# Optimization experiments

Measured on AMD Instinct MI355X. Metric: run time of the kernel, lower is better.

Reference implementation:

```python
import jax, jax.numpy as jnp
import numpy as np

EMBED = 1024
HEADS = 16
HEAD_DIM = EMBED // HEADS
NEG = -1e20


def setup_inputs() -> dict:
    key = jax.random.key(0)
    ks = jax.random.split(key, 12)
    N, S, E = 2, 2048, EMBED
    w = lambda k: (jax.random.normal(k, (E, E), dtype=jnp.float32) * 0.02)
    b = lambda k: (jax.random.normal(k, (E,), dtype=jnp.float32) * 0.02)
    return {
        "values": jax.random.normal(ks[0], (N, S, E), dtype=jnp.float32),
        "keys": jax.random.normal(ks[1], (N, S, E), dtype=jnp.float32),
        "query": jax.random.normal(ks[2], (N, S, E), dtype=jnp.float32),
        "mask": jnp.ones((N, S), dtype=jnp.int32),
        "Wv": w(ks[3]), "bv": b(ks[4]),
        "Wk": w(ks[5]), "bk": b(ks[6]),
        "Wq": w(ks[7]), "bq": b(ks[8]),
        "Wo": w(ks[9]), "bo": b(ks[10]),
    }


def reference(values, keys, query, mask, Wv, bv, Wk, bk, Wq, bq, Wo, bo):
    N, S, E = query.shape
    # torch nn.Linear: x @ W.T + b
    v = (values @ Wv.T + bv).reshape(N, S, HEADS, HEAD_DIM)
    k = (keys @ Wk.T + bk).reshape(N, S, HEADS, HEAD_DIM)
    q = (query @ Wq.T + bq).reshape(N, S, HEADS, HEAD_DIM)
    # full [N,H,Q,K] score matrix, as in the original einsum
    energy = jnp.einsum('nqhd,nkhd->nhqk', q, k)
    # 2D mask with mismatched dims triggers causal tril path in the original
    causal = jnp.tril(jnp.ones((S, S), dtype=bool))  # [Q,K]
    energy = jnp.where(causal[None, None, :, :], energy, NEG)
    # NOTE: original scales by sqrt(embed_size), not sqrt(head_dim)
    attn = jax.nn.softmax(energy / jnp.sqrt(jnp.float32(E)), axis=3)
    out = jnp.einsum('nhqk,nkhd->nqhd', attn, v).reshape(N, S, E)
    return out @ Wo.T + bo
```

## Files before the change

kernel.cpp:

```cpp
#include <hip/hip_runtime.h>

typedef __bf16 bf16;
typedef __bf16 bf16x4 __attribute__((ext_vector_type(4)));
typedef __bf16 bf16x8 __attribute__((ext_vector_type(8)));
typedef float floatx4 __attribute__((ext_vector_type(4)));

#define GLOAD_LDS16(gp, lp) \
  __builtin_amdgcn_global_load_lds( \
      (const __attribute__((address_space(1))) void*)(gp), \
      (__attribute__((address_space(3))) void*)(lp), 16, 0, 0)

__global__ __launch_bounds__(256) void cvt_all_kernel(
    const float* __restrict__ v, const float* __restrict__ k, const float* __restrict__ q,
    const float* __restrict__ wv, const float* __restrict__ wk,
    const float* __restrict__ wq, const float* __restrict__ wo,
    bf16* __restrict__ xv, bf16* __restrict__ xk, bf16* __restrict__ xq,
    bf16* __restrict__ bwv, bf16* __restrict__ bwk, bf16* __restrict__ bwq,
    bf16* __restrict__ bwo) {
  const int i = blockIdx.x * 256 + threadIdx.x;
  const int A4 = 1 << 20;
  const float* src; bf16* dst; int off;
  if (i < A4)            { src = v; dst = xv; off = i; }
  else if (i < 2 * A4)   { src = k; dst = xk; off = i - A4; }
  else if (i < 3 * A4)   { src = q; dst = xq; off = i - 2 * A4; }
  else {
    int j = i - 3 * A4; int r = j >> 18; off = j & ((1 << 18) - 1);
    src = (r == 0) ? wv : (r == 1) ? wk : (r == 2) ? wq : wo;
    dst = (r == 0) ? bwv : (r == 1) ? bwk : (r == 2) ? bwq : bwo;
  }
  float4 x = reinterpret_cast<const float4*>(src)[off];
  union { bf16 b[4]; short4 s; } u;
  u.b[0] = (bf16)x.x; u.b[1] = (bf16)x.y; u.b[2] = (bf16)x.z; u.b[3] = (bf16)x.w;
  reinterpret_cast<short4*>(dst)[off] = u.s;
}

template <int MODE>
__device__ __forceinline__ void gemm_body(
    const bf16* __restrict__ A, const bf16* __restrict__ B,
    const float* __restrict__ bias, void* __restrict__ Cout,
    int bx, int by, bf16* __restrict__ SMEM) {
  constexpr int K = 1024, N = 1024;
  constexpr int NSTEP = K / 32;
  const int tid = threadIdx.x;
  const int lane = tid & 63;
  const int wave = tid >> 6;
  const int quad = lane >> 4;
  const int l16 = lane & 15;
  const int wm = (wave >> 1) * 64;
  const int wn = (wave & 1) * 64;
  const int am0 = by * 128;
  const int bn0 = bx * 128;
  const int srow = lane >> 2;
  const int scol = (lane & 3) * 8;

  floatx4 acc[4][4] = {};

  auto stage = [&](int step, int bufsel) {
    const int k0 = step * 32;
    bf16* As = SMEM + bufsel * 8192;
    bf16* Bs = As + 4096;
#pragma unroll
    for (int j = 0; j < 2; j++) {
      const int chunk = wave * 2 + j;
      const int row = chunk * 16 + srow;
      GLOAD_LDS16(A + (size_t)(am0 + row) * K + k0 + scol, As + chunk * 512);
      GLOAD_LDS16(B + (size_t)(bn0 + row) * K + k0 + scol, Bs + chunk * 512);
    }
  };

  auto compute = [&](int bufsel) {
    const bf16* As = SMEM + bufsel * 8192;
    const bf16* Bs = As + 4096;
    bf16x8 af[4], bfv[4];
#pragma unroll
    for (int mi = 0; mi < 4; mi++)
      af[mi] = *reinterpret_cast<const bf16x8*>(&As[(wm + mi * 16 + l16) * 32 + quad * 8]);
#pragma unroll
    for (int ni = 0; ni < 4; ni++)
      bfv[ni] = *reinterpret_cast<const bf16x8*>(&Bs[(wn + ni * 16 + l16) * 32 + quad * 8]);
#pragma unroll
    for (int mi = 0; mi < 4; mi++)
#pragma unroll
      for (int ni = 0; ni < 4; ni++)
        acc[mi][ni] = __builtin_amdgcn_mfma_f32_16x16x32_bf16(af[mi], bfv[ni], acc[mi][ni], 0, 0, 0);
  };

  stage(0, 0);
  for (int t = 0; t < NSTEP; t += 2) {
    __syncthreads();
    stage(t + 1, 1);
    compute(0);
    __syncthreads();
    if (t + 2 < NSTEP) stage(t + 2, 0);
    compute(1);
  }

  if constexpr (MODE == 2) {
#pragma unroll
    for (int mi = 0; mi < 4; mi++) {
#pragma unroll
      for (int ni = 0; ni < 4; ni++) {
        const int col = bn0 + wn + ni * 16 + l16;
        const float bb = bias[col];
        const int row = am0 + wm + mi * 16 + quad * 4;
#pragma unroll
        for (int r = 0; r < 4; r++)
          reinterpret_cast<float*>(Cout)[(size_t)(row + r) * N + col] = acc[mi][ni][r] + bb;
      }
    }
  } else {
    __syncthreads();
    bf16* T = SMEM + wave * 2048;
    const int nb = (am0 + wm) >> 11;
    const int sq0 = (am0 + wm) & 2047;
    const int h = (bn0 + wn) >> 6;
    const int nh = nb * 16 + h;
    const int r8 = lane >> 3, c8 = lane & 7;

    if constexpr (MODE == 0) {
#pragma unroll
      for (int pp = 0; pp < 2; pp++) {
#pragma unroll
        for (int mm = 0; mm < 2; mm++) {
          const int mi = pp * 2 + mm;
#pragma unroll
          for (int ni = 0; ni < 4; ni++) {
            const int d = ni * 16 + l16;
            const float bc = bias[bn0 + wn + d];
#pragma unroll
            for (int r = 0; r < 4; r++) {
              const int s = mm * 16 + quad * 4 + r;
              T[s * 64 + (d & 7) + 8 * ((d >> 3) ^ (s & 7))] = (bf16)(acc[mi][ni][r] + bc);
            }
          }
        }
#pragma unroll
        for (int it = 0; it < 4; it++) {
          const int s = it * 8 + r8;
          bf16x8 vv = *reinterpret_cast<const bf16x8*>(&T[s * 64 + ((c8 ^ r8) * 8)]);
          *reinterpret_cast<bf16x8*>(
              reinterpret_cast<bf16*>(Cout) +
              ((size_t)nh * 2048 + sq0 + pp * 32 + s) * 64 + c8 * 8) = vv;
        }
      }
    } else {
#pragma unroll
      for (int pp = 0; pp < 2; pp++) {
#pragma unroll
        for (int nn = 0; nn < 2; nn++) {
          const int ni = pp * 2 + nn;
          const int dp = nn * 16 + l16;
          const float bc = bias[bn0 + wn + pp * 32 + dp];
#pragma unroll
          for (int mi = 0; mi < 4; mi++) {
#pragma unroll
            for (int r = 0; r < 4; r++) {
              const int s = mi * 16 + quad * 4 + r;
              T[dp * 64 + (s & 7) + 8 * ((s >> 3) ^ (dp & 7))] = (bf16)(acc[mi][ni][r] + bc);
            }
          }
        }
#pragma unroll
        for (int it = 0; it < 4; it++) {
          const int dp = it * 8 + r8;
          bf16x8 vv = *reinterpret_cast<const bf16x8*>(&T[dp * 64 + ((c8 ^ r8) * 8)]);
          *reinterpret_cast<bf16x8*>(
              reinterpret_cast<bf16*>(Cout) +
              ((size_t)nh * 64 + pp * 32 + dp) * 2048 + sq0 + c8 * 8) = vv;
        }
      }
    }
  }
}

__global__ __launch_bounds__(256) void gemm_qkv(
    const bf16* __restrict__ A0, const bf16* __restrict__ B0, const float* __restrict__ c0, bf16* __restrict__ C0,
    const bf16* __restrict__ A1, const bf16* __restrict__ B1, const float* __restrict__ c1, bf16* __restrict__ C1,
    const bf16* __restrict__ A2, const bf16* __restrict__ B2, const float* __restrict__ c2, bf16* __restrict__ C2) {
  extern __shared__ __align__(16) bf16 SMEM[];
  const int lin = blockIdx.x + (blockIdx.y << 3) + (blockIdx.z << 8);
  const int swz = (lin & 7) * 96 + (lin >> 3);
  const int bz = swz >> 8;
  const int by = (swz >> 3) & 31;
  const int bx = swz & 7;
  if (bz == 0)      gemm_body<0>(A0, B0, c0, C0, bx, by, SMEM);
  else if (bz == 1) gemm_body<0>(A1, B1, c1, C1, bx, by, SMEM);
  else              gemm_body<1>(A2, B2, c2, C2, bx, by, SMEM);
}

__global__ __launch_bounds__(256) void gemm_out(
    const bf16* __restrict__ A, const bf16* __restrict__ B,
    const float* __restrict__ bias, float* __restrict__ C) {
  extern __shared__ __align__(16) bf16 SMEM[];
  const int lin = blockIdx.x + (blockIdx.y << 3);
  const int swz = (lin & 7) * 32 + (lin >> 3);
  const int by = swz >> 3;
  const int bx = swz & 7;
  gemm_body<2>(A, B, bias, C, bx, by, SMEM);
}

#define S_LEN 2048
#define EMB 1024
#define QT 128
#define KTILE 64
#define SCALE2 (0.03125f * 1.44269504f)

__global__ __launch_bounds__(256) void attn_kernel(
    const bf16* __restrict__ Qh, const bf16* __restrict__ Kh,
    const bf16* __restrict__ Vt, bf16* __restrict__ O,
    float* __restrict__ Opart, float* __restrict__ lpart) {
  __shared__ __align__(16) bf16 Ks[2 * KTILE * 64];
  __shared__ __align__(16) bf16 Vs[2 * 64 * KTILE];

  const int tid = threadIdx.x;
  const int lane = tid & 63;
  const int wave = tid >> 6;
  const int quad = lane >> 4;
  const int l16 = lane & 15;
  const int wq = wave * 32;

  const int c = blockIdx.x;
  const int role = blockIdx.y;
  const int nh = c >> 3;
  const int t = c & 7;
  const int n = nh >> 4;
  const int h = nh & 15;
  int qt, kt0, kt1;
  if (role == 0) { qt = t; kt0 = 0; kt1 = 2 * t + 2; }
  else {
    qt = 15 - t;
    const int halfk = qt + 1;
    kt0 = (role == 1) ? 0 : halfk;
    kt1 = (role == 1) ? halfk : 2 * halfk;
  }
  const int q0 = qt * QT;

  bf16x8 aq[2][2];
  {
    const bf16* Qb = Qh + ((size_t)nh * S_LEN + q0 + wq + l16) * 64 + quad * 8;
#pragma unroll
    for (int mi = 0; mi < 2; mi++)
#pragma unroll
      for (int kc = 0; kc < 2; kc++)
        aq[mi][kc] = *reinterpret_cast<const bf16x8*>(Qb + mi * 16 * 64 + kc * 32);
  }

  float l_part[2] = {};
  floatx4 o_acc[2][4] = {};

  const bf16* Kbase = Kh + (size_t)nh * S_LEN * 64;
  const bf16* Vbase = Vt + (size_t)nh * 64 * S_LEN;

  const int srl = lane >> 3;
  const int sc8 = lane & 7;

  auto stage = [&](int kt) {
    const int k0s = kt * KTILE;
    const int buf = (kt & 1) * 4096;
#pragma unroll
    for (int j = 0; j < 2; j++) {
      const int rl = wave * 16 + j * 8 + srl;
      const int c8s = ((sc8 ^ (rl & 7)) * 8);
      GLOAD_LDS16(Kbase + (size_t)(k0s + rl) * 64 + c8s, Ks + buf + (wave * 16 + j * 8) * 64);
      GLOAD_LDS16(Vbase + (size_t)rl * S_LEN + k0s + c8s, Vs + buf + (wave * 16 + j * 8) * 64);
    }
  };

  stage(kt0);
  for (int kt = kt0; kt < kt1; kt++) {
    const int k0 = kt * KTILE;
    __syncthreads();
    if (kt + 1 < kt1) stage(kt + 1);
    const bf16* Kc = Ks + (kt & 1) * 4096;
    const bf16* Vc = Vs + (kt & 1) * 4096;

    floatx4 s_acc[2][4] = {};
#pragma unroll
    for (int kc = 0; kc < 2; kc++) {
      bf16x8 bk[4];
#pragma unroll
      for (int ni = 0; ni < 4; ni++)
        bk[ni] = *reinterpret_cast<const bf16x8*>(
            &Kc[(ni * 16 + l16) * 64 + (((kc * 4 + quad) ^ (l16 & 7)) * 8)]);
#pragma unroll
      for (int mi = 0; mi < 2; mi++)
#pragma unroll
        for (int ni = 0; ni < 4; ni++)
          s_acc[mi][ni] = __builtin_amdgcn_mfma_f32_16x16x32_bf16(bk[ni], aq[mi][kc], s_acc[mi][ni], 0, 0, 0);
    }

    const bool needMask = (k0 + KTILE - 1) > (q0 + wq);
    const int qg = q0 + wq + l16;
    union PU { bf16x8 w[2]; bf16x4 q[4]; };
    PU P[2];
#pragma unroll
    for (int mi = 0; mi < 2; mi++) {
#pragma unroll
      for (int ni = 0; ni < 4; ni++) {
        const int kgb = k0 + ni * 16 + quad * 4;
        bf16x4 pk;
#pragma unroll
        for (int r = 0; r < 4; r++) {
          float pr = __builtin_amdgcn_exp2f(s_acc[mi][ni][r] * SCALE2);
          if (needMask) pr = ((kgb + r) <= (qg + mi * 16)) ? pr : 0.f;
          l_part[mi] += pr;
          pk[r] = (bf16)pr;
        }
        P[mi].q[ni] = pk;
      }
    }

#pragma unroll
    for (int kc = 0; kc < 2; kc++) {
      bf16x8 bv[4];
#pragma unroll
      for (int di = 0; di < 4; di++) {
        const bf16* base = Vc + (di * 16 + l16) * 64;
        const int e = l16 & 7;
        union VU { bf16x8 v8; bf16x4 h[2]; } vu;
        vu.h[0] = *reinterpret_cast<const bf16x4*>(
            base + (((kc * 4 + (quad >> 1)) ^ e) * 8) + (quad & 1) * 4);
        vu.h[1] = *reinterpret_cast<const bf16x4*>(
            base + (((kc * 4 + 2 + (quad >> 1)) ^ e) * 8) + (quad & 1) * 4);
        bv[di] = vu.v8;
      }
#pragma unroll
      for (int mi = 0; mi < 2; mi++)
#pragma unroll
        for (int di = 0; di < 4; di++)
          o_acc[mi][di] = __builtin_amdgcn_mfma_f32_16x16x32_bf16(P[mi].w[kc], bv[di], o_acc[mi][di], 0, 0, 0);
    }
  }

  float l_sum[2];
#pragma unroll
  for (int mi = 0; mi < 2; mi++) {
    float s = l_part[mi];
    s += __shfl_xor(s, 16);
    s += __shfl_xor(s, 32);
    l_sum[mi] = s;
  }

  if (role == 0) {
    bf16* Op = O + ((size_t)(n * S_LEN + q0 + wq)) * EMB + h * 64;
#pragma unroll
    for (int mi = 0; mi < 2; mi++) {
      const float linv = 1.0f / l_sum[mi];
#pragma unroll
      for (int r = 0; r < 4; r++) {
        const float inv = __shfl(linv, quad * 4 + r);
        bf16* orow = Op + (size_t)(mi * 16 + quad * 4 + r) * EMB;
#pragma unroll
        for (int di = 0; di < 4; di++)
          orow[di * 16 + l16] = (bf16)(o_acc[mi][di][r] * inv);
      }
    }
  } else {
    float* Ob = Opart + ((size_t)c * 2 + (role - 1)) * (QT * 64);
    float* lb = lpart + ((size_t)c * 2 + (role - 1)) * QT;
#pragma unroll
    for (int mi = 0; mi < 2; mi++)
      if (lane < 16) lb[wq + mi * 16 + lane] = l_sum[mi];
#pragma unroll
    for (int mi = 0; mi < 2; mi++)
#pragma unroll
      for (int r = 0; r < 4; r++) {
        float* orow = Ob + (size_t)(wq + mi * 16 + quad * 4 + r) * 64;
#pragma unroll
        for (int di = 0; di < 4; di++)
          orow[di * 16 + l16] = o_acc[mi][di][r];
      }
  }
}

__global__ __launch_bounds__(256) void attn_combine(
    const float* __restrict__ Opart, const float* __restrict__ lpart,
    bf16* __restrict__ O) {
  const int c = blockIdx.x;
  const int nh = c >> 3;
  const int t = c & 7;
  const int qt = 15 - t;
  const int n = nh >> 4;
  const int h = nh & 15;
  const float* O1 = Opart + (size_t)c * 2 * (QT * 64);
  const float* O2 = O1 + QT * 64;
  const float* l1 = lpart + (size_t)c * 2 * QT;
  const float* l2 = l1 + QT;
  const int tid = threadIdx.x;
  for (int i = tid; i < QT * 64 / 4; i += 256) {
    const int row = i >> 4;
    const float inv = 1.0f / (l1[row] + l2[row]);
    float4 a = reinterpret_cast<const float4*>(O1)[i];
    float4 b = reinterpret_cast<const float4*>(O2)[i];
    bf16x4 pk;
    pk[0] = (bf16)((a.x + b.x) * inv);
    pk[1] = (bf16)((a.y + b.y) * inv);
    pk[2] = (bf16)((a.z + b.z) * inv);
    pk[3] = (bf16)((a.w + b.w) * inv);
    *reinterpret_cast<bf16x4*>(
        O + ((size_t)(n * S_LEN + qt * QT + row)) * EMB + h * 64 + (i & 15) * 4) = pk;
  }
}

extern "C" void kernel_launch(void* const* d_in, const int* in_sizes, int n_in,
                              void* d_out, int out_size, void* d_ws, size_t ws_size,
                              hipStream_t stream) {
  (void)in_sizes; (void)n_in; (void)out_size; (void)ws_size;
  const float* values = (const float*)d_in[0];
  const float* keys   = (const float*)d_in[1];
  const float* query  = (const float*)d_in[2];
  const float* Wv = (const float*)d_in[4];
  const float* bv = (const float*)d_in[5];
  const float* Wk = (const float*)d_in[6];
  const float* bk = (const float*)d_in[7];
  const float* Wq = (const float*)d_in[8];
  const float* bq = (const float*)d_in[9];
  const float* Wo = (const float*)d_in[10];
  const float* bo = (const float*)d_in[11];
  float* out = (float*)d_out;

  const int S = 2048, E = 1024;
  const int M = 2 * S;
  const size_t MB_ = 1u << 20;
  char* ws = (char*)d_ws;
  bf16* xv  = (bf16*)(ws + 0 * MB_);
  bf16* xk  = (bf16*)(ws + 8 * MB_);
  bf16* xq  = (bf16*)(ws + 16 * MB_);
  bf16* wvb = (bf16*)(ws + 24 * MB_);
  bf16* wkb = (bf16*)(ws + 26 * MB_);
  bf16* wqb = (bf16*)(ws + 28 * MB_);
  bf16* wob = (bf16*)(ws + 30 * MB_);
  bf16* kh  = (bf16*)(ws + 32 * MB_);
  bf16* qh  = (bf16*)(ws + 40 * MB_);
  bf16* vt  = (bf16*)(ws + 48 * MB_);
  bf16* ao  = (bf16*)(ws + 56 * MB_);
  float* Opart = (float*)(ws + 0 * MB_);
  float* lpart = (float*)(ws + 17 * MB_);

  cvt_all_kernel<<<(4 << 20) / 256, 256, 0, stream>>>(
      values, keys, query, Wv, Wk, Wq, Wo,
      xv, xk, xq, wvb, wkb, wqb, wob);

  gemm_qkv<<<dim3(E / 128, M / 128, 3), 256, 32768, stream>>>(
      xq, wqb, bq, qh,
      xk, wkb, bk, kh,
      xv, wvb, bv, vt);

  attn_kernel<<<dim3(256, 3), 256, 0, stream>>>(qh, kh, vt, ao, Opart, lpart);
  attn_combine<<<dim3(256), 256, 0, stream>>>(Opart, lpart, ao);

  gemm_out<<<dim3(E / 128, M / 128), 256, 32768, stream>>>(ao, wob, bo, out);
}
```

Measured before the change: 226.0 us.

## Fuse split-KV combine into attention and retile output GEMM to 128x64

Removes the separate attn_combine launch. Each pair of split-KV blocks now increments an atomic counter, and the second block to finish merges the partial outputs and sums into the bf16 attention output. The output projection GEMM gets its own kernel with 128x64 tiles and a 16x32 grid, giving 512 blocks instead of 256 to fill more CUs, at the cost of less operand reuse per block. The change adds a memset of the counters and threadfence-based synchronisation, which must be correct for memory visibility.

```diff
diff --git a/kernel.cpp b/kernel.cpp
--- a/kernel.cpp
+++ b/kernel.cpp
@@ -39,7 +39,7 @@
     const bf16* __restrict__ A, const bf16* __restrict__ B,
     const float* __restrict__ bias, void* __restrict__ Cout,
     int bx, int by, bf16* __restrict__ SMEM) {
-  constexpr int K = 1024, N = 1024;
+  constexpr int K = 1024;
   constexpr int NSTEP = K / 32;
   const int tid = threadIdx.x;
   const int lane = tid & 63;
@@ -95,79 +95,64 @@
     compute(1);
   }
 
-  if constexpr (MODE == 2) {
-#pragma unroll
-    for (int mi = 0; mi < 4; mi++) {
-#pragma unroll
-      for (int ni = 0; ni < 4; ni++) {
-        const int col = bn0 + wn + ni * 16 + l16;
-        const float bb = bias[col];
-        const int row = am0 + wm + mi * 16 + quad * 4;
-#pragma unroll
-        for (int r = 0; r < 4; r++)
-          reinterpret_cast<float*>(Cout)[(size_t)(row + r) * N + col] = acc[mi][ni][r] + bb;
-      }
-    }
-  } else {
-    __syncthreads();
-    bf16* T = SMEM + wave * 2048;
-    const int nb = (am0 + wm) >> 11;
-    const int sq0 = (am0 + wm) & 2047;
-    const int h = (bn0 + wn) >> 6;
-    const int nh = nb * 16 + h;
-    const int r8 = lane >> 3, c8 = lane & 7;
-
-    if constexpr (MODE == 0) {
-#pragma unroll
-      for (int pp = 0; pp < 2; pp++) {
-#pragma unroll
-        for (int mm = 0; mm < 2; mm++) {
-          const int mi = pp * 2 + mm;
-#pragma unroll
-          for (int ni = 0; ni < 4; ni++) {
-            const int d = ni * 16 + l16;
-            const float bc = bias[bn0 + wn + d];
-#pragma unroll
-            for (int r = 0; r < 4; r++) {
-              const int s = mm * 16 + quad * 4 + r;
-              T[s * 64 + (d & 7) + 8 * ((d >> 3) ^ (s & 7))] = (bf16)(acc[mi][ni][r] + bc);
-            }
+  __syncthreads();
+  bf16* T = SMEM + wave * 2048;
+  const int nb = (am0 + wm) >> 11;
+  const int sq0 = (am0 + wm) & 2047;
+  const int h = (bn0 + wn) >> 6;
+  const int nh = nb * 16 + h;
+  const int r8 = lane >> 3, c8 = lane & 7;
+
+  if constexpr (MODE == 0) {
+#pragma unroll
+    for (int pp = 0; pp < 2; pp++) {
+#pragma unroll
+      for (int mm = 0; mm < 2; mm++) {
+        const int mi = pp * 2 + mm;
+#pragma unroll
+        for (int ni = 0; ni < 4; ni++) {
+          const int d = ni * 16 + l16;
+          const float bc = bias[bn0 + wn + d];
+#pragma unroll
+          for (int r = 0; r < 4; r++) {
+            const int s = mm * 16 + quad * 4 + r;
+            T[s * 64 + (d & 7) + 8 * ((d >> 3) ^ (s & 7))] = (bf16)(acc[mi][ni][r] + bc);
           }
         }
-#pragma unroll
-        for (int it = 0; it < 4; it++) {
-          const int s = it * 8 + r8;
-          bf16x8 vv = *reinterpret_cast<const bf16x8*>(&T[s * 64 + ((c8 ^ r8) * 8)]);
-          *reinterpret_cast<bf16x8*>(
-              reinterpret_cast<bf16*>(Cout) +
-              ((size_t)nh * 2048 + sq0 + pp * 32 + s) * 64 + c8 * 8) = vv;
-        }
-      }
-    } else {
-#pragma unroll
-      for (int pp = 0; pp < 2; pp++) {
-#pragma unroll
-        for (int nn = 0; nn < 2; nn++) {
-          const int ni = pp * 2 + nn;
-          const int dp = nn * 16 + l16;
-          const float bc = bias[bn0 + wn + pp * 32 + dp];
-#pragma unroll
-          for (int mi = 0; mi < 4; mi++) {
-#pragma unroll
-            for (int r = 0; r < 4; r++) {
-              const int s = mi * 16 + quad * 4 + r;
-              T[dp * 64 + (s & 7) + 8 * ((s >> 3) ^ (dp & 7))] = (bf16)(acc[mi][ni][r] + bc);
-            }
+      }
+#pragma unroll
+      for (int it = 0; it < 4; it++) {
+        const int s = it * 8 + r8;
+        bf16x8 vv = *reinterpret_cast<const bf16x8*>(&T[s * 64 + ((c8 ^ r8) * 8)]);
+        *reinterpret_cast<bf16x8*>(
+            reinterpret_cast<bf16*>(Cout) +
+            ((size_t)nh * 2048 + sq0 + pp * 32 + s) * 64 + c8 * 8) = vv;
+      }
+    }
+  } else {
+#pragma unroll
+    for (int pp = 0; pp < 2; pp++) {
+#pragma unroll
+      for (int nn = 0; nn < 2; nn++) {
+        const int ni = pp * 2 + nn;
+        const int dp = nn * 16 + l16;
+        const float bc = bias[bn0 + wn + pp * 32 + dp];
+#pragma unroll
+        for (int mi = 0; mi < 4; mi++) {
+#pragma unroll
+          for (int r = 0; r < 4; r++) {
+            const int s = mi * 16 + quad * 4 + r;
+            T[dp * 64 + (s & 7) + 8 * ((s >> 3) ^ (dp & 7))] = (bf16)(acc[mi][ni][r] + bc);
           }
         }
-#pragma unroll
-        for (int it = 0; it < 4; it++) {
-          const int dp = it * 8 + r8;
-          bf16x8 vv = *reinterpret_cast<const bf16x8*>(&T[dp * 64 + ((c8 ^ r8) * 8)]);
-          *reinterpret_cast<bf16x8*>(
-              reinterpret_cast<bf16*>(Cout) +
-              ((size_t)nh * 64 + pp * 32 + dp) * 2048 + sq0 + c8 * 8) = vv;
-        }
+      }
+#pragma unroll
+      for (int it = 0; it < 4; it++) {
+        const int dp = it * 8 + r8;
+        bf16x8 vv = *reinterpret_cast<const bf16x8*>(&T[dp * 64 + ((c8 ^ r8) * 8)]);
+        *reinterpret_cast<bf16x8*>(
+            reinterpret_cast<bf16*>(Cout) +
+            ((size_t)nh * 64 + pp * 32 + dp) * 2048 + sq0 + c8 * 8) = vv;
       }
     }
   }
@@ -192,11 +177,81 @@
     const bf16* __restrict__ A, const bf16* __restrict__ B,
     const float* __restrict__ bias, float* __restrict__ C) {
   extern __shared__ __align__(16) bf16 SMEM[];
-  const int lin = blockIdx.x + (blockIdx.y << 3);
-  const int swz = (lin & 7) * 32 + (lin >> 3);
-  const int by = swz >> 3;
-  const int bx = swz & 7;
-  gemm_body<2>(A, B, bias, C, bx, by, SMEM);
+  constexpr int K = 1024, N = 1024;
+  constexpr int NSTEP = 32;
+  const int lin = blockIdx.x + (blockIdx.y << 4);
+  const int swz = (lin & 7) * 64 + (lin >> 3);
+  const int by = swz >> 4;
+  const int bx = swz & 15;
+  const int tid = threadIdx.x;
+  const int lane = tid & 63;
+  const int wave = tid >> 6;
+  const int quad = lane >> 4;
+  const int l16 = lane & 15;
+  const int wm = (wave >> 1) * 64;
+  const int wn = (wave & 1) * 32;
+  const int am0 = by * 128;
+  const int bn0 = bx * 64;
+  const int srow = lane >> 2;
+  const int scol = (lane & 3) * 8;
+
+  floatx4 acc[4][2] = {};
+
+  auto stage = [&](int step, int bufsel) {
+    const int k0 = step * 32;
+    bf16* As = SMEM + bufsel * 6144;
+    bf16* Bs = As + 4096;
+#pragma unroll
+    for (int j = 0; j < 2; j++) {
+      const int chunk = wave * 2 + j;
+      const int row = chunk * 16 + srow;
+      GLOAD_LDS16(A + (size_t)(am0 + row) * K + k0 + scol, As + chunk * 512);
+    }
+    {
+      const int row = wave * 16 + srow;
+      GLOAD_LDS16(B + (size_t)(bn0 + row) * K + k0 + scol, Bs + wave * 512);
+    }
+  };
+
+  auto compute = [&](int bufsel) {
+    const bf16* As = SMEM + bufsel * 6144;
+    const bf16* Bs = As + 4096;
+    bf16x8 af[4], bfv[2];
+#pragma unroll
+    for (int mi = 0; mi < 4; mi++)
+      af[mi] = *reinterpret_cast<const bf16x8*>(&As[(wm + mi * 16 + l16) * 32 + quad * 8]);
+#pragma unroll
+    for (int ni = 0; ni < 2; ni++)
+      bfv[ni] = *reinterpret_cast<const bf16x8*>(&Bs[(wn + ni * 16 + l16) * 32 + quad * 8]);
+#pragma unroll
+    for (int mi = 0; mi < 4; mi++)
+#pragma unroll
+      for (int ni = 0; ni < 2; ni++)
+        acc[mi][ni] = __builtin_amdgcn_mfma_f32_16x16x32_bf16(af[mi], bfv[ni], acc[mi][ni], 0, 0, 0);
+  };
+
+  stage(0, 0);
+  for (int t = 0; t < NSTEP; t += 2) {
+    __syncthreads();
+    stage(t + 1, 1);
+    compute(0);
+    __syncthreads();
+    if (t + 2 < NSTEP) stage(t + 2, 0);
+    compute(1);
+  }
+
+#pragma unroll
+  for (int mi = 0; mi < 4; mi++) {
+#pragma unroll
+    for (int ni = 0; ni < 2; ni++) {
+      const int col = bn0 + wn + ni * 16 + l16;
+      const float bb = bias[col];
+      const int row = am0 + wm + mi * 16 + quad * 4;
+#pragma unroll
+      for (int r = 0; r < 4; r++)
+        C[(size_t)(row + r) * N + col] = acc[mi][ni][r] + bb;
+    }
+  }
 }
 
 #define S_LEN 2048
@@ -208,9 +263,11 @@
 __global__ __launch_bounds__(256) void attn_kernel(
     const bf16* __restrict__ Qh, const bf16* __restrict__ Kh,
     const bf16* __restrict__ Vt, bf16* __restrict__ O,
-    float* __restrict__ Opart, float* __restrict__ lpart) {
+    float* __restrict__ Opart, float* __restrict__ lpart,
+    unsigned int* __restrict__ cnt) {
   __shared__ __align__(16) bf16 Ks[2 * KTILE * 64];
   __shared__ __align__(16) bf16 Vs[2 * 64 * KTILE];
+  __shared__ int who;
 
   const int tid = threadIdx.x;
   const int lane = tid & 63;
@@ -370,35 +427,33 @@
         for (int di = 0; di < 4; di++)
           orow[di * 16 + l16] = o_acc[mi][di][r];
       }
-  }
-}
-
-__global__ __launch_bounds__(256) void attn_combine(
-    const float* __restrict__ Opart, const float* __restrict__ lpart,
-    bf16* __restrict__ O) {
-  const int c = blockIdx.x;
-  const int nh = c >> 3;
-  const int t = c & 7;
-  const int qt = 15 - t;
-  const int n = nh >> 4;
-  const int h = nh & 15;
-  const float* O1 = Opart + (size_t)c * 2 * (QT * 64);
-  const float* O2 = O1 + QT * 64;
-  const float* l1 = lpart + (size_t)c * 2 * QT;
-  const float* l2 = l1 + QT;
-  const int tid = threadIdx.x;
-  for (int i = tid; i < QT * 64 / 4; i += 256) {
-    const int row = i >> 4;
-    const float inv = 1.0f / (l1[row] + l2[row]);
-    float4 a = reinterpret_cast<const float4*>(O1)[i];
-    float4 b = reinterpret_cast<const float4*>(O2)[i];
-    bf16x4 pk;
-    pk[0] = (bf16)((a.x + b.x) * inv);
-    pk[1] = (bf16)((a.y + b.y) * inv);
-    pk[2] = (bf16)((a.z + b.z) * inv);
-    pk[3] = (bf16)((a.w + b.w) * inv);
-    *reinterpret_cast<bf16x4*>(
-        O + ((size_t)(n * S_LEN + qt * QT + row)) * EMB + h * 64 + (i & 15) * 4) = pk;
+
+    __syncthreads();
+    if (tid == 0) {
+      __threadfence();
+      who = (int)atomicAdd(&cnt[c], 1u);
+    }
+    __syncthreads();
+    if (who == 1) {
+      __threadfence();
+      const float* O1 = Opart + (size_t)c * 2 * (QT * 64);
+      const float* O2 = O1 + QT * 64;
+      const float* l1 = lpart + (size_t)c * 2 * QT;
+      const float* l2 = l1 + QT;
+      for (int i = tid; i < QT * 64 / 4; i += 256) {
+        const int row = i >> 4;
+        const float inv = 1.0f / (l1[row] + l2[row]);
+        float4 a = reinterpret_cast<const float4*>(O1)[i];
+        float4 b = reinterpret_cast<const float4*>(O2)[i];
+        bf16x4 pko;
+        pko[0] = (bf16)((a.x + b.x) * inv);
+        pko[1] = (bf16)((a.y + b.y) * inv);
+        pko[2] = (bf16)((a.z + b.z) * inv);
+        pko[3] = (bf16)((a.w + b.w) * inv);
+        *reinterpret_cast<bf16x4*>(
+            O + ((size_t)(n * S_LEN + qt * QT + row)) * EMB + h * 64 + (i & 15) * 4) = pko;
+      }
+    }
   }
 }
 
@@ -436,6 +491,7 @@
   bf16* ao  = (bf16*)(ws + 56 * MB_);
   float* Opart = (float*)(ws + 0 * MB_);
   float* lpart = (float*)(ws + 17 * MB_);
+  unsigned int* cnt = (unsigned int*)(ws + 18 * MB_);
 
   cvt_all_kernel<<<(4 << 20) / 256, 256, 0, stream>>>(
       values, keys, query, Wv, Wk, Wq, Wo,
@@ -446,8 +502,9 @@
       xk, wkb, bk, kh,
       xv, wvb, bv, vt);
 
-  attn_kernel<<<dim3(256, 3), 256, 0, stream>>>(qh, kh, vt, ao, Opart, lpart);
-  attn_combine<<<dim3(256), 256, 0, stream>>>(Opart, lpart, ao);
-
-  gemm_out<<<dim3(E / 128, M / 128), 256, 32768, stream>>>(ao, wob, bo, out);
+  hipMemsetAsync(cnt, 0, 256 * sizeof(unsigned int), stream);
+
+  attn_kernel<<<dim3(256, 3), 256, 0, stream>>>(qh, kh, vt, ao, Opart, lpart, cnt);
+
+  gemm_out<<<dim3(16, 32), 256, 24576, stream>>>(ao, wob, bo, out);
 }
```

Result: slower. 265.9 us (+17.6%).
